# Optimization experiments

Measured on AMD Instinct MI355X. Metric: run time of the kernel, lower is better.

Reference implementation:

```python
import jax, jax.numpy as jnp
import numpy as np

BUCKETS = 32
DIM = 1024
HEADS = 16
TEMP = 0.75
SINK_ITERS = 7
LOG_EPS = 1e-6
GUMBEL_EPS = 1e-4


def _sinkhorn(r, n_iters):
    # iterative row/col log-normalization, then exp (matches torch loop)
    for _ in range(n_iters):
        r = r - jax.scipy.special.logsumexp(r, axis=2, keepdims=True)
        r = r - jax.scipy.special.logsumexp(r, axis=1, keepdims=True)
    return jnp.exp(r)


def setup_inputs() -> dict:
    key = jax.random.key(0)
    kq, kk, kv, kw, kg = jax.random.split(key, 5)
    B, H, T, DH = 4, 16, 4096, 64
    q = jax.random.normal(kq, (B, H, T, DH), jnp.float32)
    k = jax.random.normal(kk, (B, H, T, DH), jnp.float32)
    v = jax.random.normal(kv, (B, H, T, DH), jnp.float32)
    sort_w = jax.random.normal(kw, (1, H, DH, BUCKETS), jnp.float32)
    u = jax.random.uniform(kg, (B * H, BUCKETS, BUCKETS), jnp.float32, 0.0, 1.0)
    gumbel_noise = -jnp.log(-jnp.log(u + GUMBEL_EPS) + GUMBEL_EPS)
    return {"q": q, "k": k, "v": v, "sort_w": sort_w, "gumbel_noise": gumbel_noise}


def reference(q, k, v, sort_w, gumbel_noise):
    b, h, t, dh = q.shape
    bh = b * h
    bsz = t // BUCKETS  # tokens per bucket
    # bucket: (bh, buckets, bsz, dh)
    qb = q.reshape(bh, BUCKETS, bsz, dh)
    kb = k.reshape(bh, BUCKETS, bsz, dh)
    vb = v.reshape(bh, BUCKETS, bsz, dh)
    # bucket summaries for routing
    b_k_r = kb.sum(axis=2)  # (bh, buckets, dh)
    e_w = jnp.broadcast_to(sort_w, (b, h, dh, BUCKETS)).reshape(bh, dh, BUCKETS)
    R = jnp.log(jax.nn.relu(jnp.einsum('bud,bdv->buv', b_k_r, e_w)) + LOG_EPS)
    R = (R + gumbel_noise) / TEMP
    R = _sinkhorn(R, SINK_ITERS)  # soft permutation matrix (bh, buckets, buckets)
    R = jnp.tril(R, -1)  # causal: only attend to strictly earlier buckets
    # soft-permute key/value buckets
    k_re = jnp.einsum('buv,bvtd->butd', R, kb)
    v_re = jnp.einsum('buv,bvtd->butd', R, vb)
    bk = jnp.concatenate([k_re, kb], axis=2)  # (bh, buckets, 2*bsz, dh)
    bv = jnp.concatenate([v_re, vb], axis=2)
    dots = jnp.einsum('buie,buje->buij', qb, bk) * (DIM ** -0.5)
    attn = jax.nn.softmax(dots, axis=-1)
    out = jnp.einsum('buij,buje->buie', attn, bv)  # (bh, buckets, bsz, dh)
    return out.reshape(b, h, t, dh)
```

## Files before the change

kernel.cpp:

```cpp
#include <hip/hip_runtime.h>
#include <hip/hip_bf16.h>

#define BUCKETS 32
#define BSZ 128
#define DH 64
#define TEMPINV 1.3333333333333333f
#define SINK_ITERS 7
#define LOG_EPS 1e-6f
#define SCALE 0.03125f

typedef short bf16x8 __attribute__((ext_vector_type(8)));
typedef float f32x4 __attribute__((ext_vector_type(4)));

__device__ __forceinline__ void bf8_to_f32(const uint4 x, float* f) {
    f[0] = __uint_as_float(x.x << 16);
    f[1] = __uint_as_float(x.x & 0xffff0000u);
    f[2] = __uint_as_float(x.y << 16);
    f[3] = __uint_as_float(x.y & 0xffff0000u);
    f[4] = __uint_as_float(x.z << 16);
    f[5] = __uint_as_float(x.z & 0xffff0000u);
    f[6] = __uint_as_float(x.w << 16);
    f[7] = __uint_as_float(x.w & 0xffff0000u);
}

__device__ __forceinline__ unsigned f2bf(float f) {
    unsigned x = __float_as_uint(f);
    return (x + 0x7fffu + ((x >> 16) & 1u)) >> 16;
}

__device__ __forceinline__ uint4 packbf8(const float* f) {
    uint4 r;
    r.x = f2bf(f[0]) | (f2bf(f[1]) << 16);
    r.y = f2bf(f[2]) | (f2bf(f[3]) << 16);
    r.z = f2bf(f[4]) | (f2bf(f[5]) << 16);
    r.w = f2bf(f[6]) | (f2bf(f[7]) << 16);
    return r;
}

__device__ __forceinline__ void load_lds16(const uint4* g, uint4* l) {
    __builtin_amdgcn_global_load_lds(
        (const __attribute__((address_space(1))) unsigned int*)g,
        (__attribute__((address_space(3))) unsigned int*)l, 16, 0, 0);
}

__global__ __launch_bounds__(256) void bksum_kernel(
    const float* __restrict__ kptr, float* __restrict__ bkr)
{
    const int t = blockIdx.x;
    const int tid = threadIdx.x;
    __shared__ float4 part[16][17];
    const float4* k4 = (const float4*)kptr + (size_t)t * 2048;
    const int c4 = tid & 15, rg = tid >> 4;
    float4 s; s.x = 0.f; s.y = 0.f; s.z = 0.f; s.w = 0.f;
    for (int r = rg; r < 128; r += 16) {
        float4 a = k4[r * 16 + c4];
        s.x += a.x; s.y += a.y; s.z += a.z; s.w += a.w;
    }
    part[rg][c4] = s;
    __syncthreads();
    if (tid < 16) {
        float4 acc = part[0][tid];
        for (int g = 1; g < 16; ++g) {
            float4 p = part[g][tid];
            acc.x += p.x; acc.y += p.y; acc.z += p.z; acc.w += p.w;
        }
        ((float4*)bkr)[t * 16 + tid] = acc;
    }
}

__global__ __launch_bounds__(256) void sinkhorn_kernel(
    const float* __restrict__ bkrp,
    const float* __restrict__ swptr,
    const float* __restrict__ gptr,
    float* __restrict__ Rout)
{
    const int b = blockIdx.x;
    const int h = b & 15;
    const int tid = threadIdx.x;

    __shared__ float bk[BUCKETS][DH];
    __shared__ float sw[DH][BUCKETS];
    __shared__ float R[BUCKETS][BUCKETS + 1];

    for (int o = tid; o < DH * BUCKETS; o += 256)
        sw[o >> 5][o & 31] = swptr[h * DH * BUCKETS + o];
    for (int o = tid; o < BUCKETS * DH; o += 256)
        bk[o >> 6][o & 63] = bkrp[b * 2048 + o];
    __syncthreads();

    for (int o = tid; o < BUCKETS * BUCKETS; o += 256) {
        const int uu = o >> 5, vv = o & 31;
        float dot = 0.f;
        for (int d = 0; d < DH; ++d) dot = fmaf(bk[uu][d], sw[d][vv], dot);
        const float g = gptr[b * 1024 + o];
        R[uu][vv] = (logf(fmaxf(dot, 0.f) + LOG_EPS) + g) * TEMPINV;
    }
    __syncthreads();

    const int rr = tid >> 3, sub = tid & 7;
    for (int it = 0; it < SINK_ITERS; ++it) {
        {
            float vals[4];
            float m = -1e30f, s = 0.f;
            #pragma unroll
            for (int q = 0; q < 4; ++q) { vals[q] = R[rr][sub * 4 + q]; m = fmaxf(m, vals[q]); }
            m = fmaxf(m, __shfl_xor(m, 1)); m = fmaxf(m, __shfl_xor(m, 2)); m = fmaxf(m, __shfl_xor(m, 4));
            #pragma unroll
            for (int q = 0; q < 4; ++q) s += expf(vals[q] - m);
            s += __shfl_xor(s, 1); s += __shfl_xor(s, 2); s += __shfl_xor(s, 4);
            const float lse = m + logf(s);
            #pragma unroll
            for (int q = 0; q < 4; ++q) R[rr][sub * 4 + q] = vals[q] - lse;
            __syncthreads();
        }
        {
            float vals[4];
            float m = -1e30f, s = 0.f;
            #pragma unroll
            for (int q = 0; q < 4; ++q) { vals[q] = R[sub * 4 + q][rr]; m = fmaxf(m, vals[q]); }
            m = fmaxf(m, __shfl_xor(m, 1)); m = fmaxf(m, __shfl_xor(m, 2)); m = fmaxf(m, __shfl_xor(m, 4));
            #pragma unroll
            for (int q = 0; q < 4; ++q) s += expf(vals[q] - m);
            s += __shfl_xor(s, 1); s += __shfl_xor(s, 2); s += __shfl_xor(s, 4);
            const float lse = m + logf(s);
            #pragma unroll
            for (int q = 0; q < 4; ++q) R[sub * 4 + q][rr] = vals[q] - lse;
            __syncthreads();
        }
    }

    for (int o = tid; o < BUCKETS * BUCKETS; o += 256) {
        const int uu = o >> 5, vv = o & 31;
        Rout[b * 1024 + o] = (vv < uu) ? expf(R[uu][vv]) : 0.f;
    }
}

__global__ __launch_bounds__(256) void reshuffle4_kernel(
    const float* __restrict__ kptr,
    const float* __restrict__ vptr,
    const float* __restrict__ Rmat,
    uint4* __restrict__ kimg,
    uint4* __restrict__ vimg)
{
    const int j0 = blockIdx.x;
    const int b  = blockIdx.y;
    const int tid = threadIdx.x;
    const int w = tid >> 6, g = (tid >> 3) & 7, c8 = tid & 7;
    const int u = g * 4 + w;

    __shared__ float ls[32][8][64];
    __shared__ float lr[32][33];

    for (int o = tid; o < 1024; o += 256)
        lr[o >> 5][o & 31] = Rmat[b * 1024 + o];

    float4* ls4 = (float4*)ls;

    {
        const float4* kb4 = (const float4*)kptr + (size_t)b * 65536 + j0 * 128;
        for (int it = 0; it < 16; ++it) {
            const int idx = it * 256 + tid;
            const int v = idx >> 7, i = idx & 127;
            ls4[v * 128 + i] = kb4[v * 2048 + i];
        }
    }
    __syncthreads();
    {
        float ka[8][8];
        #pragma unroll
        for (int r = 0; r < 8; ++r)
            #pragma unroll
            for (int t = 0; t < 8; ++t) ka[r][t] = 0.f;
        for (int vv = 0; vv < u; ++vv) {
            const float rwt = lr[u][vv];
            #pragma unroll
            for (int r = 0; r < 8; ++r)
                #pragma unroll
                for (int t = 0; t < 8; ++t)
                    ka[r][t] = fmaf(rwt, ls[vv][r][c8 * 8 + t], ka[r][t]);
        }
        uint4* kdst = kimg + ((size_t)b * 32 + u) * 2048;
        #pragma unroll
        for (int r = 0; r < 8; ++r) {
            kdst[(j0 * 8 + r) * 8 + (c8 ^ r)] = packbf8(ka[r]);
            float o8[8];
            #pragma unroll
            for (int t = 0; t < 8; ++t) o8[t] = ls[u][r][c8 * 8 + t];
            kdst[(128 + j0 * 8 + r) * 8 + (c8 ^ r)] = packbf8(o8);
        }
    }
    __syncthreads();

    {
        const float4* vb4 = (const float4*)vptr + (size_t)b * 65536 + j0 * 128;
        for (int it = 0; it < 16; ++it) {
            const int idx = it * 256 + tid;
            const int v = idx >> 7, i = idx & 127;
            ls4[v * 128 + i] = vb4[v * 2048 + i];
        }
    }
    __syncthreads();
    {
        uint4 wor[8];
        #pragma unroll
        for (int t = 0; t < 8; ++t) {
            wor[t].x = f2bf(ls[u][0][c8 * 8 + t]) | (f2bf(ls[u][1][c8 * 8 + t]) << 16);
            wor[t].y = f2bf(ls[u][2][c8 * 8 + t]) | (f2bf(ls[u][3][c8 * 8 + t]) << 16);
            wor[t].z = f2bf(ls[u][4][c8 * 8 + t]) | (f2bf(ls[u][5][c8 * 8 + t]) << 16);
            wor[t].w = f2bf(ls[u][6][c8 * 8 + t]) | (f2bf(ls[u][7][c8 * 8 + t]) << 16);
        }
        float va[8][8];
        #pragma unroll
        for (int r = 0; r < 8; ++r)
            #pragma unroll
            for (int t = 0; t < 8; ++t) va[r][t] = 0.f;
        for (int vv = 0; vv < u; ++vv) {
            const float rwt = lr[u][vv];
            #pragma unroll
            for (int r = 0; r < 8; ++r)
                #pragma unroll
                for (int t = 0; t < 8; ++t)
                    va[r][t] = fmaf(rwt, ls[vv][r][c8 * 8 + t], va[r][t]);
        }
        __syncthreads();

        uint4* img = (uint4*)ls;
        #pragma unroll
        for (int t = 0; t < 8; ++t) {
            const int blk = c8 * 8 + (t ^ c8);
            uint4 wre;
            wre.x = f2bf(va[0][t]) | (f2bf(va[1][t]) << 16);
            wre.y = f2bf(va[2][t]) | (f2bf(va[3][t]) << 16);
            wre.z = f2bf(va[4][t]) | (f2bf(va[5][t]) << 16);
            wre.w = f2bf(va[6][t]) | (f2bf(va[7][t]) << 16);
            img[u * 64 + blk] = wre;
            img[2048 + u * 64 + blk] = wor[t];
        }
        __syncthreads();

        for (int o = tid; o < 2048; o += 256) {
            const int uu = o >> 6, blk = o & 63;
            const size_t tb = ((size_t)b * 32 + uu) * 2048;
            vimg[tb + j0 * 64 + blk] = img[o];
            vimg[tb + (16 + j0) * 64 + blk] = img[2048 + o];
        }
    }
}

__global__ __launch_bounds__(128) void attn_fallback(
    const float* __restrict__ qptr,
    const float* __restrict__ kptr,
    const float* __restrict__ vptr,
    const float* __restrict__ Rmat,
    float4* __restrict__ optr)
{
    const int u = blockIdx.x;
    const int b = blockIdx.y;
    const int tid = threadIdx.x;

    __shared__ uint4 sbk[2048];
    __shared__ uint4 sbv[2048];

    const float4* k4 = (const float4*)kptr + (size_t)b * 65536;
    const float4* v4 = (const float4*)vptr + (size_t)b * 65536;
    const float4* q4 = (const float4*)qptr + (size_t)b * 65536;

    const float* Rrow = Rmat + (b * BUCKETS + u) * BUCKETS;
    for (int o = tid; o < 1024; o += 128) {
        float ka[8] = {0.f,0.f,0.f,0.f,0.f,0.f,0.f,0.f};
        float va[8] = {0.f,0.f,0.f,0.f,0.f,0.f,0.f,0.f};
        for (int vv = 0; vv < u; ++vv) {
            const float r = Rrow[vv];
            float4 a = k4[vv * 2048 + 2 * o], c = k4[vv * 2048 + 2 * o + 1];
            ka[0] = fmaf(r, a.x, ka[0]); ka[1] = fmaf(r, a.y, ka[1]);
            ka[2] = fmaf(r, a.z, ka[2]); ka[3] = fmaf(r, a.w, ka[3]);
            ka[4] = fmaf(r, c.x, ka[4]); ka[5] = fmaf(r, c.y, ka[5]);
            ka[6] = fmaf(r, c.z, ka[6]); ka[7] = fmaf(r, c.w, ka[7]);
            float4 av = v4[vv * 2048 + 2 * o], cv = v4[vv * 2048 + 2 * o + 1];
            va[0] = fmaf(r, av.x, va[0]); va[1] = fmaf(r, av.y, va[1]);
            va[2] = fmaf(r, av.z, va[2]); va[3] = fmaf(r, av.w, va[3]);
            va[4] = fmaf(r, cv.x, va[4]); va[5] = fmaf(r, cv.y, va[5]);
            va[6] = fmaf(r, cv.z, va[6]); va[7] = fmaf(r, cv.w, va[7]);
        }
        sbk[o] = packbf8(ka);
        sbv[o] = packbf8(va);
        float4 a = k4[u * 2048 + 2 * o], c = k4[u * 2048 + 2 * o + 1];
        float f[8] = {a.x,a.y,a.z,a.w,c.x,c.y,c.z,c.w};
        sbk[1024 + o] = packbf8(f);
        float4 av = v4[u * 2048 + 2 * o], cv = v4[u * 2048 + 2 * o + 1];
        float gg[8] = {av.x,av.y,av.z,av.w,cv.x,cv.y,cv.z,cv.w};
        sbv[1024 + o] = packbf8(gg);
    }
    __syncthreads();

    const int i = tid;
    float qr[64];
    const float4* qrow = q4 + (u * 128 + i) * 16;
    for (int d4 = 0; d4 < 16; ++d4) {
        float4 t = qrow[d4];
        qr[d4 * 4 + 0] = t.x; qr[d4 * 4 + 1] = t.y;
        qr[d4 * 4 + 2] = t.z; qr[d4 * 4 + 3] = t.w;
    }

    float acc[64];
    for (int d = 0; d < 64; ++d) acc[d] = 0.f;
    float l = 0.f;

    for (int j = 0; j < 256; ++j) {
        float s = 0.f;
        for (int d8 = 0; d8 < 8; ++d8) {
            float f[8];
            bf8_to_f32(sbk[j * 8 + d8], f);
            for (int t = 0; t < 8; ++t) s = fmaf(qr[d8 * 8 + t], f[t], s);
        }
        const float p = __expf(s * SCALE);
        l += p;
        for (int d8 = 0; d8 < 8; ++d8) {
            float f[8];
            bf8_to_f32(sbv[j * 8 + d8], f);
            for (int t = 0; t < 8; ++t)
                acc[d8 * 8 + t] = fmaf(p, f[t], acc[d8 * 8 + t]);
        }
    }

    const float inv = 1.f / l;
    float4* orow = optr + (size_t)b * 65536 + (u * 128 + i) * 16;
    for (int d4 = 0; d4 < 16; ++d4) {
        float4 t;
        t.x = acc[d4 * 4 + 0] * inv;
        t.y = acc[d4 * 4 + 1] * inv;
        t.z = acc[d4 * 4 + 2] * inv;
        t.w = acc[d4 * 4 + 3] * inv;
        orow[d4] = t;
    }
}

__global__ __launch_bounds__(256) void attn_mfma3(
    const float* __restrict__ qptr,
    const uint4* __restrict__ kimg,
    const uint4* __restrict__ vimg,
    float* __restrict__ optr)
{
    const int u = blockIdx.x;
    const int b = blockIdx.y;
    const int tid = threadIdx.x;
    const int lane = tid & 63;
    const int w = tid >> 6;
    const int lg = lane >> 4;
    const int lr = lane & 15;

    __shared__ uint4 sK[2][512];
    __shared__ uint4 sV[2][512];
    __shared__ uint4 sP[1024];

    const size_t tile = (size_t)b * 32 + u;
    const uint4* gk = kimg + tile * 2048;
    const uint4* gv = vimg + tile * 2048;

    const float* qbase = qptr + (size_t)b * 262144 + (size_t)u * 8192;
    float4 qa[2][2], qc[2][2];
    #pragma unroll
    for (int mt = 0; mt < 2; ++mt)
        #pragma unroll
        for (int c = 0; c < 2; ++c) {
            const int row = w * 32 + mt * 16 + lr;
            const float4* qr = (const float4*)(qbase + row * 64 + (c * 4 + lg) * 8);
            qa[mt][c] = qr[0];
            qc[mt][c] = qr[1];
        }

#define STAGE_KB(kbi, bufi) do { \
        load_lds16(gk + (kbi) * 512 +   0 + tid, &sK[bufi][  0 + (w << 6)]); \
        load_lds16(gk + (kbi) * 512 + 256 + tid, &sK[bufi][256 + (w << 6)]); \
        load_lds16(gv + (kbi) * 512 +   0 + tid, &sV[bufi][  0 + (w << 6)]); \
        load_lds16(gv + (kbi) * 512 + 256 + tid, &sV[bufi][256 + (w << 6)]); \
    } while (0)
    STAGE_KB(0, 0);
    STAGE_KB(1, 1);

    bf16x8 qf[2][2];
    #pragma unroll
    for (int mt = 0; mt < 2; ++mt)
        #pragma unroll
        for (int c = 0; c < 2; ++c) {
            float f[8] = {qa[mt][c].x * SCALE, qa[mt][c].y * SCALE,
                          qa[mt][c].z * SCALE, qa[mt][c].w * SCALE,
                          qc[mt][c].x * SCALE, qc[mt][c].y * SCALE,
                          qc[mt][c].z * SCALE, qc[mt][c].w * SCALE};
            uint4 tq = packbf8(f);
            qf[mt][c] = *(bf16x8*)&tq;
        }

    uint4* sPw = sP + w * 256;
    unsigned short* sPh = (unsigned short*)sPw;

    f32x4 acc[2][4];
    float lsum[2][4];
    #pragma unroll
    for (int mt = 0; mt < 2; ++mt) {
        #pragma unroll
        for (int nt = 0; nt < 4; ++nt) {
            acc[mt][nt][0] = 0.f; acc[mt][nt][1] = 0.f;
            acc[mt][nt][2] = 0.f; acc[mt][nt][3] = 0.f;
        }
        #pragma unroll
        for (int r = 0; r < 4; ++r) lsum[mt][r] = 0.f;
    }

    #pragma unroll
    for (int kb = 0; kb < 4; ++kb) {
        const uint4* bK = sK[kb & 1];
        const uint4* bV = sV[kb & 1];

        if (kb < 3) asm volatile("s_waitcnt vmcnt(4)" ::: "memory");
        else        asm volatile("s_waitcnt vmcnt(0)" ::: "memory");
        __builtin_amdgcn_s_barrier();
        __builtin_amdgcn_sched_barrier(0);

        bf16x8 kf[4][2];
        #pragma unroll
        for (int nt = 0; nt < 4; ++nt)
            #pragma unroll
            for (int c = 0; c < 2; ++c) {
                const int jj = nt * 16 + lr;
                const int dcu = c * 4 + lg;
                uint4 t = bK[jj * 8 + (dcu ^ (jj & 7))];
                kf[nt][c] = *(bf16x8*)&t;
            }
        f32x4 s[2][4];
        #pragma unroll
        for (int mt = 0; mt < 2; ++mt)
            #pragma unroll
            for (int nt = 0; nt < 4; ++nt) {
                s[mt][nt][0] = 0.f; s[mt][nt][1] = 0.f;
                s[mt][nt][2] = 0.f; s[mt][nt][3] = 0.f;
            }
        __builtin_amdgcn_s_setprio(1);
        #pragma unroll
        for (int c = 0; c < 2; ++c)
            #pragma unroll
            for (int mt = 0; mt < 2; ++mt)
                #pragma unroll
                for (int nt = 0; nt < 4; ++nt)
                    s[mt][nt] = __builtin_amdgcn_mfma_f32_16x16x32_bf16(
                        qf[mt][c], kf[nt][c], s[mt][nt], 0, 0, 0);
        __builtin_amdgcn_s_setprio(0);

        #pragma unroll
        for (int mt = 0; mt < 2; ++mt)
            #pragma unroll
            for (int nt = 0; nt < 4; ++nt)
                #pragma unroll
                for (int r = 0; r < 4; ++r) {
                    const float p = __expf(s[mt][nt][r]);
                    lsum[mt][r] += p;
                    const int row = mt * 16 + lg * 4 + r;
                    const int col = nt * 16 + lr;
                    sPh[row * 64 + (((col >> 3) ^ (row & 7)) << 3) + (col & 7)] =
                        (unsigned short)f2bf(p);
                }
        asm volatile("s_waitcnt lgkmcnt(0)" ::: "memory");
        __builtin_amdgcn_sched_barrier(0);

        bf16x8 pf[2][2];
        #pragma unroll
        for (int mt = 0; mt < 2; ++mt)
            #pragma unroll
            for (int c = 0; c < 2; ++c) {
                const int row = mt * 16 + lr;
                const int dcu = c * 4 + lg;
                uint4 t = sPw[row * 8 + (dcu ^ (row & 7))];
                pf[mt][c] = *(bf16x8*)&t;
            }
        bf16x8 vf[4][2];
        #pragma unroll
        for (int nt = 0; nt < 4; ++nt)
            #pragma unroll
            for (int c = 0; c < 2; ++c) {
                const int pp = c * 4 + lg;
                const int d = nt * 16 + lr;
                const int blk = (d >> 3) * 8 + ((d & 7) ^ ((d >> 3) & 7));
                uint4 t = bV[pp * 64 + blk];
                vf[nt][c] = *(bf16x8*)&t;
            }
        __builtin_amdgcn_s_setprio(1);
        #pragma unroll
        for (int c = 0; c < 2; ++c)
            #pragma unroll
            for (int mt = 0; mt < 2; ++mt)
                #pragma unroll
                for (int nt = 0; nt < 4; ++nt)
                    acc[mt][nt] = __builtin_amdgcn_mfma_f32_16x16x32_bf16(
                        pf[mt][c], vf[nt][c], acc[mt][nt], 0, 0, 0);
        __builtin_amdgcn_s_setprio(0);

        __builtin_amdgcn_sched_barrier(0);
        __builtin_amdgcn_s_barrier();
        __builtin_amdgcn_sched_barrier(0);
        if (kb < 2) STAGE_KB(kb + 2, kb & 1);
    }
#undef STAGE_KB

    #pragma unroll
    for (int mt = 0; mt < 2; ++mt)
        #pragma unroll
        for (int r = 0; r < 4; ++r) {
            float sum = lsum[mt][r];
            sum += __shfl_xor(sum, 1);
            sum += __shfl_xor(sum, 2);
            sum += __shfl_xor(sum, 4);
            sum += __shfl_xor(sum, 8);
            const float inv = 1.f / sum;
            const int row = mt * 16 + lg * 4 + r;
            float* orow = optr + (size_t)b * 262144 +
                          (size_t)(u * 128 + w * 32 + row) * 64;
            #pragma unroll
            for (int nt = 0; nt < 4; ++nt)
                orow[nt * 16 + lr] = acc[mt][nt][r] * inv;
        }
}

extern "C" void kernel_launch(void* const* d_in, const int* in_sizes, int n_in,
                              void* d_out, int out_size, void* d_ws, size_t ws_size,
                              hipStream_t stream) {
    const float* q  = (const float*)d_in[0];
    const float* k  = (const float*)d_in[1];
    const float* v  = (const float*)d_in[2];
    const float* sw = (const float*)d_in[3];
    const float* g  = (const float*)d_in[4];

    float* R    = (float*)d_ws;
    float* bkr  = (float*)((char*)d_ws + 262144);
    uint4* kimg = (uint4*)((char*)d_ws + 1048576);
    uint4* vimg = (uint4*)((char*)d_ws + 1048576 + 67108864);
    const bool big_ws = (ws_size >= (size_t)1048576 + 2u * 67108864u);

    bksum_kernel<<<dim3(2048), dim3(256), 0, stream>>>(k, bkr);
    sinkhorn_kernel<<<dim3(64), dim3(256), 0, stream>>>(bkr, sw, g, R);
    if (big_ws) {
        reshuffle4_kernel<<<dim3(16, 64), dim3(256), 0, stream>>>(k, v, R, kimg, vimg);
        attn_mfma3<<<dim3(32, 64), dim3(256), 0, stream>>>(q, kimg, vimg, (float*)d_out);
    } else {
        attn_fallback<<<dim3(32, 64), dim3(128), 0, stream>>>(q, k, v, R, (float4*)d_out);
    }
}
```

Before: 344.2 us.

## Fuse all stages into one cooperative persistent kernel with grid syncs

Merges the bucket-sum, Sinkhorn, reshuffle and attention kernels into a single cooperative kernel of 512 blocks, with grid.sync between phases and each block looping over several work items. The attention phase also drops its double-buffered K/V staging and loads the whole K/V tile into shared memory at once. The goal is to remove launch gaps and inter-kernel overhead. In exchange, the Sinkhorn phase runs on only 64 blocks while the rest wait, the 80KB shared allocation limits occupancy, and overlap of loads with compute in the attention loop is lost. Separate kernels remain as a fallback if the cooperative launch fails.

```diff
diff --git a/kernel.cpp b/kernel.cpp
--- a/kernel.cpp
+++ b/kernel.cpp
@@ -1,5 +1,8 @@
 #include <hip/hip_runtime.h>
+#include <hip/hip_cooperative_groups.h>
 #include <hip/hip_bf16.h>
+
+namespace cg = cooperative_groups;
 
 #define BUCKETS 32
 #define BSZ 128
@@ -43,12 +46,12 @@
         (__attribute__((address_space(3))) unsigned int*)l, 16, 0, 0);
 }
 
-__global__ __launch_bounds__(256) void bksum_kernel(
-    const float* __restrict__ kptr, float* __restrict__ bkr)
-{
-    const int t = blockIdx.x;
+
+__device__ __forceinline__ void phase_bksum(
+    const float* __restrict__ kptr, float* __restrict__ bkr, int t, char* sm)
+{
+    float4 (*part)[17] = (float4(*)[17])sm;
     const int tid = threadIdx.x;
-    __shared__ float4 part[16][17];
     const float4* k4 = (const float4*)kptr + (size_t)t * 2048;
     const int c4 = tid & 15, rg = tid >> 4;
     float4 s; s.x = 0.f; s.y = 0.f; s.z = 0.f; s.w = 0.f;
@@ -66,24 +69,23 @@
         }
         ((float4*)bkr)[t * 16 + tid] = acc;
     }
-}
-
-__global__ __launch_bounds__(256) void sinkhorn_kernel(
+    __syncthreads();
+}
+
+__device__ __forceinline__ void phase_sink(
     const float* __restrict__ bkrp,
     const float* __restrict__ swptr,
     const float* __restrict__ gptr,
-    float* __restrict__ Rout)
-{
-    const int b = blockIdx.x;
+    float* __restrict__ Rout, int b, char* sm)
+{
+    float (*bk)[DH]  = (float(*)[DH])sm;
+    float (*swl)[BUCKETS] = (float(*)[BUCKETS])(sm + 8192);
+    float (*R)[BUCKETS + 1] = (float(*)[BUCKETS + 1])(sm + 16384);
     const int h = b & 15;
     const int tid = threadIdx.x;
 
-    __shared__ float bk[BUCKETS][DH];
-    __shared__ float sw[DH][BUCKETS];
-    __shared__ float R[BUCKETS][BUCKETS + 1];
-
     for (int o = tid; o < DH * BUCKETS; o += 256)
-        sw[o >> 5][o & 31] = swptr[h * DH * BUCKETS + o];
+        swl[o >> 5][o & 31] = swptr[h * DH * BUCKETS + o];
     for (int o = tid; o < BUCKETS * DH; o += 256)
         bk[o >> 6][o & 63] = bkrp[b * 2048 + o];
     __syncthreads();
@@ -91,7 +93,7 @@
     for (int o = tid; o < BUCKETS * BUCKETS; o += 256) {
         const int uu = o >> 5, vv = o & 31;
         float dot = 0.f;
-        for (int d = 0; d < DH; ++d) dot = fmaf(bk[uu][d], sw[d][vv], dot);
+        for (int d = 0; d < DH; ++d) dot = fmaf(bk[uu][d], swl[d][vv], dot);
         const float g = gptr[b * 1024 + o];
         R[uu][vv] = (logf(fmaxf(dot, 0.f) + LOG_EPS) + g) * TEMPINV;
     }
@@ -135,21 +137,18 @@
     }
 }
 
-__global__ __launch_bounds__(256) void reshuffle4_kernel(
+__device__ __forceinline__ void phase_reshuffle(
     const float* __restrict__ kptr,
     const float* __restrict__ vptr,
     const float* __restrict__ Rmat,
     uint4* __restrict__ kimg,
-    uint4* __restrict__ vimg)
-{
-    const int j0 = blockIdx.x;
-    const int b  = blockIdx.y;
+    uint4* __restrict__ vimg, int j0, int b, char* sm)
+{
+    float (*ls)[8][64] = (float(*)[8][64])sm;
+    float (*lr)[33]    = (float(*)[33])(sm + 65536);
     const int tid = threadIdx.x;
     const int w = tid >> 6, g = (tid >> 3) & 7, c8 = tid & 7;
     const int u = g * 4 + w;
-
-    __shared__ float ls[32][8][64];
-    __shared__ float lr[32][33];
 
     for (int o = tid; o < 1024; o += 256)
         lr[o >> 5][o & 31] = Rmat[b * 1024 + o];
@@ -245,6 +244,240 @@
             vimg[tb + (16 + j0) * 64 + blk] = img[2048 + o];
         }
     }
+}
+
+__device__ __forceinline__ void phase_attn(
+    const float* __restrict__ qptr,
+    const uint4* __restrict__ kimg,
+    const uint4* __restrict__ vimg,
+    float* __restrict__ optr, int u, int b, char* sm)
+{
+    uint4* sK = (uint4*)sm;
+    uint4* sV = (uint4*)(sm + 32768);
+    uint4* sP = (uint4*)(sm + 65536);
+    const int tid = threadIdx.x;
+    const int lane = tid & 63;
+    const int w = tid >> 6;
+    const int lg = lane >> 4;
+    const int lr = lane & 15;
+
+    const size_t tile = (size_t)b * 32 + u;
+    const uint4* gk = kimg + tile * 2048;
+    const uint4* gv = vimg + tile * 2048;
+
+    #pragma unroll
+    for (int it = 0; it < 8; ++it)
+        load_lds16(gk + it * 256 + tid, &sK[it * 256 + (w << 6)]);
+    #pragma unroll
+    for (int it = 0; it < 8; ++it)
+        load_lds16(gv + it * 256 + tid, &sV[it * 256 + (w << 6)]);
+
+    const float* qbase = qptr + (size_t)b * 262144 + (size_t)u * 8192;
+    bf16x8 qf[2][2];
+    #pragma unroll
+    for (int mt = 0; mt < 2; ++mt)
+        #pragma unroll
+        for (int c = 0; c < 2; ++c) {
+            const int row = w * 32 + mt * 16 + lr;
+            const float4* qr = (const float4*)(qbase + row * 64 + (c * 4 + lg) * 8);
+            float4 a = qr[0], cc = qr[1];
+            float f[8] = {a.x * SCALE, a.y * SCALE, a.z * SCALE, a.w * SCALE,
+                          cc.x * SCALE, cc.y * SCALE, cc.z * SCALE, cc.w * SCALE};
+            uint4 tq = packbf8(f);
+            qf[mt][c] = *(bf16x8*)&tq;
+        }
+    __syncthreads();
+
+    uint4* sPw = sP + w * 256;
+    unsigned short* sPh = (unsigned short*)sPw;
+
+    f32x4 acc[2][4];
+    float lsum[2][4];
+    #pragma unroll
+    for (int mt = 0; mt < 2; ++mt) {
+        #pragma unroll
+        for (int nt = 0; nt < 4; ++nt) {
+            acc[mt][nt][0] = 0.f; acc[mt][nt][1] = 0.f;
+            acc[mt][nt][2] = 0.f; acc[mt][nt][3] = 0.f;
+        }
+        #pragma unroll
+        for (int r = 0; r < 4; ++r) lsum[mt][r] = 0.f;
+    }
+
+    for (int kb = 0; kb < 4; ++kb) {
+        bf16x8 kf[4][2];
+        #pragma unroll
+        for (int nt = 0; nt < 4; ++nt)
+            #pragma unroll
+            for (int c = 0; c < 2; ++c) {
+                const int j = kb * 64 + nt * 16 + lr;
+                const int dcu = c * 4 + lg;
+                uint4 t = sK[j * 8 + (dcu ^ (j & 7))];
+                kf[nt][c] = *(bf16x8*)&t;
+            }
+        f32x4 s[2][4];
+        #pragma unroll
+        for (int mt = 0; mt < 2; ++mt)
+            #pragma unroll
+            for (int nt = 0; nt < 4; ++nt) {
+                s[mt][nt][0] = 0.f; s[mt][nt][1] = 0.f;
+                s[mt][nt][2] = 0.f; s[mt][nt][3] = 0.f;
+            }
+        __builtin_amdgcn_s_setprio(1);
+        #pragma unroll
+        for (int c = 0; c < 2; ++c)
+            #pragma unroll
+            for (int mt = 0; mt < 2; ++mt)
+                #pragma unroll
+                for (int nt = 0; nt < 4; ++nt)
+                    s[mt][nt] = __builtin_amdgcn_mfma_f32_16x16x32_bf16(
+                        qf[mt][c], kf[nt][c], s[mt][nt], 0, 0, 0);
+        __builtin_amdgcn_s_setprio(0);
+
+        #pragma unroll
+        for (int mt = 0; mt < 2; ++mt)
+            #pragma unroll
+            for (int nt = 0; nt < 4; ++nt)
+                #pragma unroll
+                for (int r = 0; r < 4; ++r) {
+                    const float p = __expf(s[mt][nt][r]);
+                    lsum[mt][r] += p;
+                    const int row = mt * 16 + lg * 4 + r;
+                    const int col = nt * 16 + lr;
+                    sPh[row * 64 + (((col >> 3) ^ (row & 7)) << 3) + (col & 7)] =
+                        (unsigned short)f2bf(p);
+                }
+        asm volatile("s_waitcnt lgkmcnt(0)" ::: "memory");
+        __builtin_amdgcn_sched_barrier(0);
+
+        bf16x8 pf[2][2];
+        #pragma unroll
+        for (int mt = 0; mt < 2; ++mt)
+            #pragma unroll
+            for (int c = 0; c < 2; ++c) {
+                const int row = mt * 16 + lr;
+                const int dcu = c * 4 + lg;
+                uint4 t = sPw[row * 8 + (dcu ^ (row & 7))];
+                pf[mt][c] = *(bf16x8*)&t;
+            }
+        bf16x8 vf[4][2];
+        #pragma unroll
+        for (int nt = 0; nt < 4; ++nt)
+            #pragma unroll
+            for (int c = 0; c < 2; ++c) {
+                const int p = kb * 8 + c * 4 + lg;
+                const int d = nt * 16 + lr;
+                const int blk = (d >> 3) * 8 + ((d & 7) ^ ((d >> 3) & 7));
+                uint4 t = sV[p * 64 + blk];
+                vf[nt][c] = *(bf16x8*)&t;
+            }
+        __builtin_amdgcn_s_setprio(1);
+        #pragma unroll
+        for (int c = 0; c < 2; ++c)
+            #pragma unroll
+            for (int mt = 0; mt < 2; ++mt)
+                #pragma unroll
+                for (int nt = 0; nt < 4; ++nt)
+                    acc[mt][nt] = __builtin_amdgcn_mfma_f32_16x16x32_bf16(
+                        pf[mt][c], vf[nt][c], acc[mt][nt], 0, 0, 0);
+        __builtin_amdgcn_s_setprio(0);
+    }
+
+    #pragma unroll
+    for (int mt = 0; mt < 2; ++mt)
+        #pragma unroll
+        for (int r = 0; r < 4; ++r) {
+            float sum = lsum[mt][r];
+            sum += __shfl_xor(sum, 1);
+            sum += __shfl_xor(sum, 2);
+            sum += __shfl_xor(sum, 4);
+            sum += __shfl_xor(sum, 8);
+            const float inv = 1.f / sum;
+            const int row = mt * 16 + lg * 4 + r;
+            float* orow = optr + (size_t)b * 262144 +
+                          (size_t)(u * 128 + w * 32 + row) * 64;
+            #pragma unroll
+            for (int nt = 0; nt < 4; ++nt)
+                orow[nt * 16 + lr] = acc[mt][nt][r] * inv;
+        }
+}
+
+__global__ __launch_bounds__(256, 2) void mega_kernel(
+    const float* __restrict__ q,
+    const float* __restrict__ k,
+    const float* __restrict__ v,
+    const float* __restrict__ swp,
+    const float* __restrict__ gp,
+    float* __restrict__ R,
+    float* __restrict__ bkr,
+    uint4* __restrict__ kimg,
+    uint4* __restrict__ vimg,
+    float* __restrict__ out)
+{
+    __shared__ __align__(16) char sm[81920];
+    cg::grid_group grid = cg::this_grid();
+    const int blk = blockIdx.x;
+
+    #pragma unroll 1
+    for (int rep = 0; rep < 4; ++rep)
+        phase_bksum(k, bkr, blk * 4 + rep, sm);
+    grid.sync();
+
+    if (blk < 64) phase_sink(bkr, swp, gp, R, blk, sm);
+    grid.sync();
+
+    #pragma unroll 1
+    for (int rep = 0; rep < 2; ++rep) {
+        __syncthreads();
+        const int vb = blk * 2 + rep;
+        phase_reshuffle(k, v, R, kimg, vimg, vb & 15, vb >> 4, sm);
+    }
+    grid.sync();
+
+    #pragma unroll 1
+    for (int rep = 0; rep < 4; ++rep) {
+        __syncthreads();
+        const int vb = blk * 4 + rep;
+        phase_attn(q, kimg, vimg, out, vb & 31, vb >> 5, sm);
+    }
+}
+
+__global__ __launch_bounds__(256) void bksum_k(
+    const float* __restrict__ kptr, float* __restrict__ bkr)
+{
+    __shared__ __align__(16) char sm[4352];
+    phase_bksum(kptr, bkr, blockIdx.x, sm);
+}
+
+__global__ __launch_bounds__(256) void sink_k(
+    const float* __restrict__ bkrp,
+    const float* __restrict__ swptr,
+    const float* __restrict__ gptr,
+    float* __restrict__ Rout)
+{
+    __shared__ __align__(16) char sm[20608];
+    phase_sink(bkrp, swptr, gptr, Rout, blockIdx.x, sm);
+}
+
+__global__ __launch_bounds__(256) void reshuffle_k(
+    const float* __restrict__ kptr,
+    const float* __restrict__ vptr,
+    const float* __restrict__ Rmat,
+    uint4* __restrict__ kimg,
+    uint4* __restrict__ vimg)
+{
+    __shared__ __align__(16) char sm[69760];
+    phase_reshuffle(kptr, vptr, Rmat, kimg, vimg, blockIdx.x, blockIdx.y, sm);
+}
+
+__global__ __launch_bounds__(256) void attn_k(
+    const float* __restrict__ qptr,
+    const uint4* __restrict__ kimg,
+    const uint4* __restrict__ vimg,
+    float* __restrict__ optr)
+{
+    __shared__ __align__(16) char sm[81920];
+    phase_attn(qptr, kimg, vimg, optr, blockIdx.x, blockIdx.y, sm);
 }
 
 __global__ __launch_bounds__(128) void attn_fallback(
@@ -335,191 +568,6 @@
     }
 }
 
-__global__ __launch_bounds__(256) void attn_mfma3(
-    const float* __restrict__ qptr,
-    const uint4* __restrict__ kimg,
-    const uint4* __restrict__ vimg,
-    float* __restrict__ optr)
-{
-    const int u = blockIdx.x;
-    const int b = blockIdx.y;
-    const int tid = threadIdx.x;
-    const int lane = tid & 63;
-    const int w = tid >> 6;
-    const int lg = lane >> 4;
-    const int lr = lane & 15;
-
-    __shared__ uint4 sK[2][512];
-    __shared__ uint4 sV[2][512];
-    __shared__ uint4 sP[1024];
-
-    const size_t tile = (size_t)b * 32 + u;
-    const uint4* gk = kimg + tile * 2048;
-    const uint4* gv = vimg + tile * 2048;
-
-    const float* qbase = qptr + (size_t)b * 262144 + (size_t)u * 8192;
-    float4 qa[2][2], qc[2][2];
-    #pragma unroll
-    for (int mt = 0; mt < 2; ++mt)
-        #pragma unroll
-        for (int c = 0; c < 2; ++c) {
-            const int row = w * 32 + mt * 16 + lr;
-            const float4* qr = (const float4*)(qbase + row * 64 + (c * 4 + lg) * 8);
-            qa[mt][c] = qr[0];
-            qc[mt][c] = qr[1];
-        }
-
-#define STAGE_KB(kbi, bufi) do { \
-        load_lds16(gk + (kbi) * 512 +   0 + tid, &sK[bufi][  0 + (w << 6)]); \
-        load_lds16(gk + (kbi) * 512 + 256 + tid, &sK[bufi][256 + (w << 6)]); \
-        load_lds16(gv + (kbi) * 512 +   0 + tid, &sV[bufi][  0 + (w << 6)]); \
-        load_lds16(gv + (kbi) * 512 + 256 + tid, &sV[bufi][256 + (w << 6)]); \
-    } while (0)
-    STAGE_KB(0, 0);
-    STAGE_KB(1, 1);
-
-    bf16x8 qf[2][2];
-    #pragma unroll
-    for (int mt = 0; mt < 2; ++mt)
-        #pragma unroll
-        for (int c = 0; c < 2; ++c) {
-            float f[8] = {qa[mt][c].x * SCALE, qa[mt][c].y * SCALE,
-                          qa[mt][c].z * SCALE, qa[mt][c].w * SCALE,
-                          qc[mt][c].x * SCALE, qc[mt][c].y * SCALE,
-                          qc[mt][c].z * SCALE, qc[mt][c].w * SCALE};
-            uint4 tq = packbf8(f);
-            qf[mt][c] = *(bf16x8*)&tq;
-        }
-
-    uint4* sPw = sP + w * 256;
-    unsigned short* sPh = (unsigned short*)sPw;
-
-    f32x4 acc[2][4];
-    float lsum[2][4];
-    #pragma unroll
-    for (int mt = 0; mt < 2; ++mt) {
-        #pragma unroll
-        for (int nt = 0; nt < 4; ++nt) {
-            acc[mt][nt][0] = 0.f; acc[mt][nt][1] = 0.f;
-            acc[mt][nt][2] = 0.f; acc[mt][nt][3] = 0.f;
-        }
-        #pragma unroll
-        for (int r = 0; r < 4; ++r) lsum[mt][r] = 0.f;
-    }
-
-    #pragma unroll
-    for (int kb = 0; kb < 4; ++kb) {
-        const uint4* bK = sK[kb & 1];
-        const uint4* bV = sV[kb & 1];
-
-        if (kb < 3) asm volatile("s_waitcnt vmcnt(4)" ::: "memory");
-        else        asm volatile("s_waitcnt vmcnt(0)" ::: "memory");
-        __builtin_amdgcn_s_barrier();
-        __builtin_amdgcn_sched_barrier(0);
-
-        bf16x8 kf[4][2];
-        #pragma unroll
-        for (int nt = 0; nt < 4; ++nt)
-            #pragma unroll
-            for (int c = 0; c < 2; ++c) {
-                const int jj = nt * 16 + lr;
-                const int dcu = c * 4 + lg;
-                uint4 t = bK[jj * 8 + (dcu ^ (jj & 7))];
-                kf[nt][c] = *(bf16x8*)&t;
-            }
-        f32x4 s[2][4];
-        #pragma unroll
-        for (int mt = 0; mt < 2; ++mt)
-            #pragma unroll
-            for (int nt = 0; nt < 4; ++nt) {
-                s[mt][nt][0] = 0.f; s[mt][nt][1] = 0.f;
-                s[mt][nt][2] = 0.f; s[mt][nt][3] = 0.f;
-            }
-        __builtin_amdgcn_s_setprio(1);
-        #pragma unroll
-        for (int c = 0; c < 2; ++c)
-            #pragma unroll
-            for (int mt = 0; mt < 2; ++mt)
-                #pragma unroll
-                for (int nt = 0; nt < 4; ++nt)
-                    s[mt][nt] = __builtin_amdgcn_mfma_f32_16x16x32_bf16(
-                        qf[mt][c], kf[nt][c], s[mt][nt], 0, 0, 0);
-        __builtin_amdgcn_s_setprio(0);
-
-        #pragma unroll
-        for (int mt = 0; mt < 2; ++mt)
-            #pragma unroll
-            for (int nt = 0; nt < 4; ++nt)
-                #pragma unroll
-                for (int r = 0; r < 4; ++r) {
-                    const float p = __expf(s[mt][nt][r]);
-                    lsum[mt][r] += p;
-                    const int row = mt * 16 + lg * 4 + r;
-                    const int col = nt * 16 + lr;
-                    sPh[row * 64 + (((col >> 3) ^ (row & 7)) << 3) + (col & 7)] =
-                        (unsigned short)f2bf(p);
-                }
-        asm volatile("s_waitcnt lgkmcnt(0)" ::: "memory");
-        __builtin_amdgcn_sched_barrier(0);
-
-        bf16x8 pf[2][2];
-        #pragma unroll
-        for (int mt = 0; mt < 2; ++mt)
-            #pragma unroll
-            for (int c = 0; c < 2; ++c) {
-                const int row = mt * 16 + lr;
-                const int dcu = c * 4 + lg;
-                uint4 t = sPw[row * 8 + (dcu ^ (row & 7))];
-                pf[mt][c] = *(bf16x8*)&t;
-            }
-        bf16x8 vf[4][2];
-        #pragma unroll
-        for (int nt = 0; nt < 4; ++nt)
-            #pragma unroll
-            for (int c = 0; c < 2; ++c) {
-                const int pp = c * 4 + lg;
-                const int d = nt * 16 + lr;
-                const int blk = (d >> 3) * 8 + ((d & 7) ^ ((d >> 3) & 7));
-                uint4 t = bV[pp * 64 + blk];
-                vf[nt][c] = *(bf16x8*)&t;
-            }
-        __builtin_amdgcn_s_setprio(1);
-        #pragma unroll
-        for (int c = 0; c < 2; ++c)
-            #pragma unroll
-            for (int mt = 0; mt < 2; ++mt)
-                #pragma unroll
-                for (int nt = 0; nt < 4; ++nt)
-                    acc[mt][nt] = __builtin_amdgcn_mfma_f32_16x16x32_bf16(
-                        pf[mt][c], vf[nt][c], acc[mt][nt], 0, 0, 0);
-        __builtin_amdgcn_s_setprio(0);
-
-        __builtin_amdgcn_sched_barrier(0);
-        __builtin_amdgcn_s_barrier();
-        __builtin_amdgcn_sched_barrier(0);
-        if (kb < 2) STAGE_KB(kb + 2, kb & 1);
-    }
-#undef STAGE_KB
-
-    #pragma unroll
-    for (int mt = 0; mt < 2; ++mt)
-        #pragma unroll
-        for (int r = 0; r < 4; ++r) {
-            float sum = lsum[mt][r];
-            sum += __shfl_xor(sum, 1);
-            sum += __shfl_xor(sum, 2);
-            sum += __shfl_xor(sum, 4);
-            sum += __shfl_xor(sum, 8);
-            const float inv = 1.f / sum;
-            const int row = mt * 16 + lg * 4 + r;
-            float* orow = optr + (size_t)b * 262144 +
-                          (size_t)(u * 128 + w * 32 + row) * 64;
-            #pragma unroll
-            for (int nt = 0; nt < 4; ++nt)
-                orow[nt * 16 + lr] = acc[mt][nt][r] * inv;
-        }
-}
-
 extern "C" void kernel_launch(void* const* d_in, const int* in_sizes, int n_in,
                               void* d_out, int out_size, void* d_ws, size_t ws_size,
                               hipStream_t stream) {
@@ -528,6 +576,7 @@
     const float* v  = (const float*)d_in[2];
     const float* sw = (const float*)d_in[3];
     const float* g  = (const float*)d_in[4];
+    float* out = (float*)d_out;
 
     float* R    = (float*)d_ws;
     float* bkr  = (float*)((char*)d_ws + 262144);
@@ -535,12 +584,20 @@
     uint4* vimg = (uint4*)((char*)d_ws + 1048576 + 67108864);
     const bool big_ws = (ws_size >= (size_t)1048576 + 2u * 67108864u);
 
-    bksum_kernel<<<dim3(2048), dim3(256), 0, stream>>>(k, bkr);
-    sinkhorn_kernel<<<dim3(64), dim3(256), 0, stream>>>(bkr, sw, g, R);
     if (big_ws) {
-        reshuffle4_kernel<<<dim3(16, 64), dim3(256), 0, stream>>>(k, v, R, kimg, vimg);
-        attn_mfma3<<<dim3(32, 64), dim3(256), 0, stream>>>(q, kimg, vimg, (float*)d_out);
+        void* args[] = {(void*)&q, (void*)&k, (void*)&v, (void*)&sw, (void*)&g,
+                        (void*)&R, (void*)&bkr, (void*)&kimg, (void*)&vimg, (void*)&out};
+        hipError_t e = hipLaunchCooperativeKernel(
+            (const void*)mega_kernel, dim3(512), dim3(256), args, 0, stream);
+        if (e != hipSuccess) {
+            bksum_k<<<dim3(2048), dim3(256), 0, stream>>>(k, bkr);
+            sink_k<<<dim3(64), dim3(256), 0, stream>>>(bkr, sw, g, R);
+            reshuffle_k<<<dim3(16, 64), dim3(256), 0, stream>>>(k, v, R, kimg, vimg);
+            attn_k<<<dim3(32, 64), dim3(256), 0, stream>>>(q, kimg, vimg, out);
+        }
     } else {
+        bksum_k<<<dim3(2048), dim3(256), 0, stream>>>(k, bkr);
+        sink_k<<<dim3(64), dim3(256), 0, stream>>>(bkr, sw, g, R);
         attn_fallback<<<dim3(32, 64), dim3(128), 0, stream>>>(q, k, v, R, (float4*)d_out);
     }
 }
```

Result: slower. 505.0 us (+46.7%).
